# Optimization experiments

Measured on AMD Instinct MI355X. Metric: run time of the kernel, lower is better.

## Reference

```python
import jax, jax.numpy as jnp
import numpy as np
from jax import lax

EPS = 1e-5  # torch BatchNorm2d default


def setup_inputs() -> dict:
    key = jax.random.key(0)
    k1, k2 = jax.random.split(key)
    x = jax.random.normal(k1, (8, 32, 28, 28), dtype=jnp.float32)
    # AdderConv.param: [out_channel, in_channel, k, k], init ~ N(0,1)
    W = jax.random.normal(k2, (64, 32, 3, 3), dtype=jnp.float32)
    # BatchNorm2d affine params at init
    gamma = jnp.ones((64,), dtype=jnp.float32)
    beta = jnp.zeros((64,), dtype=jnp.float32)
    return {"x": x, "W": W, "gamma": gamma, "beta": beta}


def _adder(patches, Wc):
    # patches: [N, K, Ho, Wo] with K = C*kh*kw (channel-major, matching torch unfold)
    # Wc: [O, K]
    # AdderNet: out[n,o,ho,wo] = -sum_k |patches[n,k,ho,wo] - Wc[o,k]|
    diff = patches[:, None, :, :, :] - Wc[None, :, :, None, None]  # [N,O,K,Ho,Wo]
    return -jnp.abs(diff).sum(axis=2)  # [N,O,Ho,Wo]


def reference(x, W, gamma, beta):
    O, C, kh, kw = W.shape
    # im2col, same layout as torch.nn.functional.unfold: feature dim = C*kh*kw
    patches = lax.conv_general_dilated_patches(
        x, (kh, kw), window_strides=(1, 1), padding=[(1, 1), (1, 1)]
    )  # [N, C*kh*kw, Ho, Wo]
    Wc = W.reshape(O, C * kh * kw)
    out = _adder(patches, Wc)  # [N, O, Ho, Wo]
    # BatchNorm2d, training mode (batch statistics, biased variance)
    mean = out.mean(axis=(0, 2, 3), keepdims=True)
    var = out.var(axis=(0, 2, 3), keepdims=True)
    y = (out - mean) * lax.rsqrt(var + EPS)
    return y * gamma[None, :, None, None] + beta[None, :, None, None]
```

## Files before the change

### kernel.cpp

```cpp
#include <hip/hip_runtime.h>

#define NB   8
#define CIN  32
#define HH   28
#define WW   28
#define OC   64
#define HWSZ (HH*WW)
#define TOTAL (NB*OC*HWSZ)
#define CNT  (NB*HWSZ)

#define TROWS 4
#define TCOLS 32
#define TSZ  (CIN*TROWS*TCOLS)

#define NCOPY 32
#define GRID  (NB*14*8)

__global__ __launch_bounds__(512) void adder_stats_kernel(
    const float* __restrict__ x, const float* __restrict__ Wt,
    float* __restrict__ raw, double* __restrict__ Sbuf)
{
    __shared__ float xs[TSZ];
    const int t     = threadIdx.x;
    const int bid   = blockIdx.x;
    const int chgrp = bid & 7;
    const int sp    = bid >> 3;
    const int rp    = sp % 14;
    const int n     = sp / 14;
    const int h0    = rp * 2;
    const int copy  = sp & (NCOPY-1);

    #pragma unroll
    for (int i = t; i < TSZ; i += 512) {
        int cc  = i >> 7;
        int r   = (i >> 5) & 3;
        int col = i & 31;
        int hh  = h0 - 1 + r;
        int ww  = col - 1;
        float v = 0.0f;
        if (hh >= 0 && hh < HH && (unsigned)ww < (unsigned)WW)
            v = x[((n*CIN + cc)*HH + hh)*WW + ww];
        xs[i] = v;
    }
    __syncthreads();

    const int lane   = t & 63;
    const int w      = __builtin_amdgcn_readfirstlane(t >> 6);
    const int khalf  = w & 1;
    const int chpair = w >> 1;
    const bool valid = lane < 56;
    const int p      = valid ? lane : 0;
    const int pr     = p / WW;
    const int pw     = p % WW;
    const int o_base = chgrp*8 + chpair*2;
    const int b0     = pr*TCOLS + pw;
    const int c0     = khalf * 16;

    float acc0 = 0.0f, acc1 = 0.0f;

    #pragma unroll 4
    for (int k = 0; k < 16; ++k) {
        const int cc = c0 + k;
        float xr[9];
        #pragma unroll
        for (int dr = 0; dr < 3; ++dr)
            #pragma unroll
            for (int dc = 0; dc < 3; ++dc)
                xr[dr*3+dc] = xs[(cc << 7) + b0 + (dr << 5) + dc];
        const float* wp0 = Wt + ((o_base    )*CIN + cc)*9;
        const float* wp1 = Wt + ((o_base + 1)*CIN + cc)*9;
        #pragma unroll
        for (int j = 0; j < 9; ++j) acc0 += __builtin_fabsf(xr[j] - wp0[j]);
        #pragma unroll
        for (int j = 0; j < 9; ++j) acc1 += __builtin_fabsf(xr[j] - wp1[j]);
    }

    __syncthreads();
    if (khalf == 1 && valid) {
        xs[chpair*112 +      lane] = acc0;
        xs[chpair*112 + 56 + lane] = acc1;
    }
    __syncthreads();

    if (khalf == 0) {
        if (valid) {
            acc0 += xs[chpair*112 +      lane];
            acc1 += xs[chpair*112 + 56 + lane];
        }
        float v0 = valid ? -acc0 : 0.0f;
        float v1 = valid ? -acc1 : 0.0f;

        if (valid) {
            const int base = (h0 + pr)*WW + pw;
            raw[(n*OC + o_base    )*HWSZ + base] = v0;
            raw[(n*OC + o_base + 1)*HWSZ + base] = v1;
        }

        float s0 = v0, q0 = v0*v0, s1 = v1, q1 = v1*v1;
        #pragma unroll
        for (int off = 32; off >= 1; off >>= 1) {
            s0 += __shfl_xor(s0, off, 64);
            q0 += __shfl_xor(q0, off, 64);
            s1 += __shfl_xor(s1, off, 64);
            q1 += __shfl_xor(q1, off, 64);
        }
        if (lane == 0) {
            double* Sc = Sbuf + copy*128;
            atomicAdd(&Sc[     o_base    ], (double)s0);
            atomicAdd(&Sc[64 + o_base    ], (double)q0);
            atomicAdd(&Sc[     o_base + 1], (double)s1);
            atomicAdd(&Sc[64 + o_base + 1], (double)q1);
        }
    }
}

__global__ __launch_bounds__(256) void bn_kernel(
    const float* __restrict__ raw, const double* __restrict__ Sbuf,
    const float* __restrict__ gamma, const float* __restrict__ beta,
    float* __restrict__ out)
{
    const int no = blockIdx.x;
    const int o  = no & (OC - 1);
    double S = 0.0, S2 = 0.0;
    #pragma unroll
    for (int k = 0; k < NCOPY; ++k) {
        S  += Sbuf[k*128 + o];
        S2 += Sbuf[k*128 + 64 + o];
    }
    double mean = S  * (1.0 / CNT);
    double var  = S2 * (1.0 / CNT) - mean * mean;
    double gs   = (double)gamma[o] / sqrt(var + 1e-5);
    const float scl = (float)gs;
    const float sh  = (float)((double)beta[o] - mean * gs);

    const int t = threadIdx.x;
    if (t < HWSZ/4) {
        float4 a = ((const float4*)raw)[no*(HWSZ/4) + t];
        float4 v;
        v.x = a.x * scl + sh;
        v.y = a.y * scl + sh;
        v.z = a.z * scl + sh;
        v.w = a.w * scl + sh;
        ((float4*)out)[no*(HWSZ/4) + t] = v;
    }
}

extern "C" void kernel_launch(void* const* d_in, const int* in_sizes, int n_in,
                              void* d_out, int out_size, void* d_ws, size_t ws_size,
                              hipStream_t stream) {
    const float* x     = (const float*)d_in[0];
    const float* Wt    = (const float*)d_in[1];
    const float* gamma = (const float*)d_in[2];
    const float* beta  = (const float*)d_in[3];
    float* out = (float*)d_out;

    double* Sbuf = (double*)d_ws;
    float*  raw  = (float*)((char*)d_ws + NCOPY*128*sizeof(double));

    hipMemsetAsync(d_ws, 0, NCOPY*128*sizeof(double), stream);
    adder_stats_kernel<<<GRID, 512, 0, stream>>>(x, Wt, raw, Sbuf);
    bn_kernel<<<NB*OC, 256, 0, stream>>>(raw, Sbuf, gamma, beta, out);
}
```

Baseline: 80.74 us.

## Preload weights into registers via readlane, drop memset and double atomics

Each wave now loads its weight slice into VGPRs once and broadcasts individual values with readlane, instead of issuing scalar global weight loads inside the inner loop. The k-split goes from 2 to 4 waves, with each wave covering 4 output channels, and the partial sums are reduced through shared memory. Per-block partial statistics are written to distinct slots, with no double atomics, so the memset launch goes away. The BN kernel reduces the 112 partials with wave shuffles. The cost is more readlane instructions and more shared-memory reduction traffic.

```diff
diff --git a/kernel.cpp b/kernel.cpp
--- a/kernel.cpp
+++ b/kernel.cpp
@@ -13,8 +13,12 @@
 #define TCOLS 32
 #define TSZ  (CIN*TROWS*TCOLS)
 
-#define NCOPY 32
-#define GRID  (NB*14*8)
+#define NSP  (NB*14)
+#define GRID (NSP*8)
+
+__device__ __forceinline__ float rl(float v, int l) {
+    return __int_as_float(__builtin_amdgcn_readlane(__float_as_int(v), l));
+}
 
 __global__ __launch_bounds__(512) void adder_stats_kernel(
     const float* __restrict__ x, const float* __restrict__ Wt,
@@ -28,7 +32,20 @@
     const int rp    = sp % 14;
     const int n     = sp / 14;
     const int h0    = rp * 2;
-    const int copy  = sp & (NCOPY-1);
+
+    const int lane  = t & 63;
+    const int w     = __builtin_amdgcn_readfirstlane(t >> 6);
+    const int kq    = w & 3;
+    const int cp    = w >> 2;
+    const int o_base = chgrp*8 + cp*4;
+
+    float vw0[4], vw1[4];
+    #pragma unroll
+    for (int r = 0; r < 4; ++r) {
+        const int run = (o_base + r)*(CIN*9) + kq*72;
+        vw0[r] = Wt[run + lane];
+        vw1[r] = Wt[run + 64 + (lane & 7)];
+    }
 
     #pragma unroll
     for (int i = t; i < TSZ; i += 512) {
@@ -36,80 +53,71 @@
         int r   = (i >> 5) & 3;
         int col = i & 31;
         int hh  = h0 - 1 + r;
-        int ww  = col - 1;
+        int ww2 = col - 1;
         float v = 0.0f;
-        if (hh >= 0 && hh < HH && (unsigned)ww < (unsigned)WW)
-            v = x[((n*CIN + cc)*HH + hh)*WW + ww];
+        if (hh >= 0 && hh < HH && (unsigned)ww2 < (unsigned)WW)
+            v = x[((n*CIN + cc)*HH + hh)*WW + ww2];
         xs[i] = v;
     }
     __syncthreads();
 
-    const int lane   = t & 63;
-    const int w      = __builtin_amdgcn_readfirstlane(t >> 6);
-    const int khalf  = w & 1;
-    const int chpair = w >> 1;
     const bool valid = lane < 56;
-    const int p      = valid ? lane : 0;
-    const int pr     = p / WW;
-    const int pw     = p % WW;
-    const int o_base = chgrp*8 + chpair*2;
-    const int b0     = pr*TCOLS + pw;
-    const int c0     = khalf * 16;
+    const int p  = valid ? lane : 0;
+    const int pr = p / WW;
+    const int pw = p % WW;
+    const int b0 = pr*TCOLS + pw;
 
-    float acc0 = 0.0f, acc1 = 0.0f;
+    float acc[4] = {0.f, 0.f, 0.f, 0.f};
 
-    #pragma unroll 4
-    for (int k = 0; k < 16; ++k) {
-        const int cc = c0 + k;
+    #pragma unroll
+    for (int k = 0; k < 8; ++k) {
+        const int cc = kq*8 + k;
         float xr[9];
         #pragma unroll
         for (int dr = 0; dr < 3; ++dr)
             #pragma unroll
             for (int dc = 0; dc < 3; ++dc)
                 xr[dr*3+dc] = xs[(cc << 7) + b0 + (dr << 5) + dc];
-        const float* wp0 = Wt + ((o_base    )*CIN + cc)*9;
-        const float* wp1 = Wt + ((o_base + 1)*CIN + cc)*9;
         #pragma unroll
-        for (int j = 0; j < 9; ++j) acc0 += __builtin_fabsf(xr[j] - wp0[j]);
-        #pragma unroll
-        for (int j = 0; j < 9; ++j) acc1 += __builtin_fabsf(xr[j] - wp1[j]);
+        for (int r = 0; r < 4; ++r) {
+            #pragma unroll
+            for (int j = 0; j < 9; ++j) {
+                const int e = k*9 + j;
+                const float wv = (e < 64) ? rl(vw0[r], e) : rl(vw1[r], e - 64);
+                acc[r] += __builtin_fabsf(xr[j] - wv);
+            }
+        }
     }
 
     __syncthreads();
-    if (khalf == 1 && valid) {
-        xs[chpair*112 +      lane] = acc0;
-        xs[chpair*112 + 56 + lane] = acc1;
+    if (kq != 0 && valid) {
+        #pragma unroll
+        for (int r = 0; r < 4; ++r)
+            xs[((kq-1)*8 + cp*4 + r)*56 + lane] = acc[r];
     }
     __syncthreads();
 
-    if (khalf == 0) {
-        if (valid) {
-            acc0 += xs[chpair*112 +      lane];
-            acc1 += xs[chpair*112 + 56 + lane];
-        }
-        float v0 = valid ? -acc0 : 0.0f;
-        float v1 = valid ? -acc1 : 0.0f;
-
-        if (valid) {
-            const int base = (h0 + pr)*WW + pw;
-            raw[(n*OC + o_base    )*HWSZ + base] = v0;
-            raw[(n*OC + o_base + 1)*HWSZ + base] = v1;
-        }
-
-        float s0 = v0, q0 = v0*v0, s1 = v1, q1 = v1*v1;
+    if (kq == 0) {
+        const int base = (h0 + pr)*WW + pw;
         #pragma unroll
-        for (int off = 32; off >= 1; off >>= 1) {
-            s0 += __shfl_xor(s0, off, 64);
-            q0 += __shfl_xor(q0, off, 64);
-            s1 += __shfl_xor(s1, off, 64);
-            q1 += __shfl_xor(q1, off, 64);
-        }
-        if (lane == 0) {
-            double* Sc = Sbuf + copy*128;
-            atomicAdd(&Sc[     o_base    ], (double)s0);
-            atomicAdd(&Sc[64 + o_base    ], (double)q0);
-            atomicAdd(&Sc[     o_base + 1], (double)s1);
-            atomicAdd(&Sc[64 + o_base + 1], (double)q1);
+        for (int r = 0; r < 4; ++r) {
+            if (valid)
+                acc[r] += xs[(     cp*4 + r)*56 + lane]
+                        + xs[( 8 + cp*4 + r)*56 + lane]
+                        + xs[(16 + cp*4 + r)*56 + lane];
+            float v = valid ? -acc[r] : 0.0f;
+            if (valid)
+                raw[(n*OC + o_base + r)*HWSZ + base] = v;
+            float s = v, q = v*v;
+            #pragma unroll
+            for (int off = 32; off >= 1; off >>= 1) {
+                s += __shfl_xor(s, off, 64);
+                q += __shfl_xor(q, off, 64);
+            }
+            if (lane == 0) {
+                Sbuf[sp*128 +      o_base + r] = (double)s;
+                Sbuf[sp*128 + 64 + o_base + r] = (double)q;
+            }
         }
     }
 }
@@ -119,21 +127,37 @@
     const float* __restrict__ gamma, const float* __restrict__ beta,
     float* __restrict__ out)
 {
+    __shared__ double dsum[4];
+    __shared__ float  sb[2];
     const int no = blockIdx.x;
     const int o  = no & (OC - 1);
-    double S = 0.0, S2 = 0.0;
-    #pragma unroll
-    for (int k = 0; k < NCOPY; ++k) {
-        S  += Sbuf[k*128 + o];
-        S2 += Sbuf[k*128 + 64 + o];
+    const int t  = threadIdx.x;
+
+    if (t < 128) {
+        double s = 0.0, q = 0.0;
+        if (t < NSP) {
+            s = Sbuf[t*128 +      o];
+            q = Sbuf[t*128 + 64 + o];
+        }
+        #pragma unroll
+        for (int off = 32; off >= 1; off >>= 1) {
+            s += __shfl_xor(s, off, 64);
+            q += __shfl_xor(q, off, 64);
+        }
+        if ((t & 63) == 0) { dsum[t>>6] = s; dsum[2 + (t>>6)] = q; }
     }
-    double mean = S  * (1.0 / CNT);
-    double var  = S2 * (1.0 / CNT) - mean * mean;
-    double gs   = (double)gamma[o] / sqrt(var + 1e-5);
-    const float scl = (float)gs;
-    const float sh  = (float)((double)beta[o] - mean * gs);
-
-    const int t = threadIdx.x;
+    __syncthreads();
+    if (t == 0) {
+        double S  = dsum[0] + dsum[1];
+        double S2 = dsum[2] + dsum[3];
+        double mean = S  * (1.0 / CNT);
+        double var  = S2 * (1.0 / CNT) - mean * mean;
+        double gs   = (double)gamma[o] / sqrt(var + 1e-5);
+        sb[0] = (float)gs;
+        sb[1] = (float)((double)beta[o] - mean * gs);
+    }
+    __syncthreads();
+    const float scl = sb[0], sh = sb[1];
     if (t < HWSZ/4) {
         float4 a = ((const float4*)raw)[no*(HWSZ/4) + t];
         float4 v;
@@ -155,9 +179,8 @@
     float* out = (float*)d_out;
 
     double* Sbuf = (double*)d_ws;
-    float*  raw  = (float*)((char*)d_ws + NCOPY*128*sizeof(double));
+    float*  raw  = (float*)((char*)d_ws + 131072);
 
-    hipMemsetAsync(d_ws, 0, NCOPY*128*sizeof(double), stream);
     adder_stats_kernel<<<GRID, 512, 0, stream>>>(x, Wt, raw, Sbuf);
     bn_kernel<<<NB*OC, 256, 0, stream>>>(raw, Sbuf, gamma, beta, out);
 }
```

Measured after the change: 79.16 us. About the same (-2.0%).
